# Optimization experiments

Hardware: AMD Instinct MI355X
Metric: run time of the kernel (lower is better)

Reference implementation:

```python
import jax, jax.numpy as jnp
import numpy as np
from jax import lax

N_LINKS = 3000
N_PATHS = 15000
PATH_LEN = 8   # max_len = max(sequences)+1
DL = 16        # link_state_dim
DP = 16        # path_state_dim
RU = 128       # readout_units
OUT = 1
T = 3


def gru_cell(x, h, k, rk, b):
    # keras GRUCell (reset_after=False): kernel [in,3u], recurrent [u,3u], bias [3u]
    gx = x @ k
    gh = h @ rk
    xz, xr, xh = jnp.split(gx, 3, axis=-1)
    hz, hr, hh = jnp.split(gh, 3, axis=-1)
    bz, br, bh = jnp.split(b, 3)
    z = jax.nn.sigmoid(xz + hz + bz)
    r = jax.nn.sigmoid(xr + hr + br)
    c = jnp.tanh(xh + r * hh + bh)
    return z * h + (1.0 - z) * c


def setup_inputs() -> dict:
    key = jax.random.key(0)
    ks = jax.random.split(key, 12)
    s = 0.1
    E = N_PATHS * PATH_LEN
    links = jax.random.randint(ks[0], (E,), 0, N_LINKS, dtype=jnp.int32)
    paths = jnp.repeat(jnp.arange(N_PATHS, dtype=jnp.int32), PATH_LEN)      # sorted, as segment_sum requires
    sequences = jnp.tile(jnp.arange(PATH_LEN, dtype=jnp.int32), N_PATHS)    # position of link on its path
    link_capacity = jax.random.uniform(ks[1], (N_LINKS,), dtype=jnp.float32) * 9.0 + 1.0
    traffic = jax.random.uniform(ks[2], (N_PATHS,), dtype=jnp.float32)
    mask_param = jax.random.normal(ks[3], (N_LINKS, N_PATHS), dtype=jnp.float32) * s  # 'explain_mask'
    path_kernel = jax.random.normal(ks[4], (DL, 3 * DP), dtype=jnp.float32) * s
    path_rec = jax.random.normal(ks[5], (DP, 3 * DP), dtype=jnp.float32) * s
    path_bias = jnp.zeros((3 * DP,), dtype=jnp.float32)
    edge_kernel = jax.random.normal(ks[6], (DP, 3 * DL), dtype=jnp.float32) * s
    edge_rec = jax.random.normal(ks[7], (DL, 3 * DL), dtype=jnp.float32) * s
    edge_bias = jnp.zeros((3 * DL,), dtype=jnp.float32)
    w1 = jax.random.normal(ks[8], (DP, RU), dtype=jnp.float32) * s
    b1 = jnp.zeros((RU,), dtype=jnp.float32)
    w2 = jax.random.normal(ks[9], (RU, RU), dtype=jnp.float32) * s
    b2 = jnp.zeros((RU,), dtype=jnp.float32)
    w3 = jax.random.normal(ks[10], (RU, OUT), dtype=jnp.float32) * s
    b3 = jnp.zeros((OUT,), dtype=jnp.float32)
    return {"links": links, "paths": paths, "sequences": sequences,
            "link_capacity": link_capacity, "traffic": traffic, "mask_param": mask_param,
            "path_kernel": path_kernel, "path_rec": path_rec, "path_bias": path_bias,
            "edge_kernel": edge_kernel, "edge_rec": edge_rec, "edge_bias": edge_bias,
            "w1": w1, "b1": b1, "w2": w2, "b2": b2, "w3": w3, "b3": b3}


def _inner_call(mask, links, paths, sequences, link_capacity, traffic,
                pk, pr, pb, ek, er, eb, w1, b1, w2, b2, w3, b3):
    link_state = jnp.concatenate([link_capacity[:, None], jnp.zeros((N_LINKS, DL - 1))], axis=1)
    path_state = jnp.concatenate([traffic[:, None], jnp.zeros((N_PATHS, DP - 1))], axis=1)
    mask_gathered = mask[links, paths]  # gather_nd -> [E]
    lens = jax.ops.segment_sum(jnp.ones_like(paths), paths, num_segments=N_PATHS)  # [n_paths]
    ts = jnp.arange(PATH_LEN)
    for _ in range(T):
        h_tild = link_state[links] * mask_gathered[:, None]                        # [E, DL]
        # scatter_nd into ragged per-path sequences: [n_paths, max_len, DL]
        link_inputs = jnp.zeros((N_PATHS, PATH_LEN, DL)).at[paths, sequences].add(h_tild)

        def step(h, xt):
            x, t = xt
            hn = gru_cell(x, h, pk, pr, pb)
            valid = (t < lens)[:, None]
            hn = jnp.where(valid, hn, h)               # freeze state past sequence_length
            return hn, jnp.where(valid, hn, 0.0)       # dynamic_rnn zeroes padded outputs

        path_state, outs = lax.scan(step, path_state, (jnp.swapaxes(link_inputs, 0, 1), ts))
        outs = jnp.swapaxes(outs, 0, 1)                # [n_paths, max_len, DP]
        m = outs[paths, sequences]                     # gather_nd -> [E, DP]
        m = jax.ops.segment_sum(m, links, num_segments=N_LINKS)  # unsorted_segment_sum
        link_state = gru_cell(m, link_state, ek, er, eb)
    # readout (dropout inactive at inference)
    h = jax.nn.selu(path_state @ w1 + b1)
    h = jax.nn.selu(h @ w2 + b2)
    r = h @ w3 + b3
    return r, mask_gathered


def reference(links, paths, sequences, link_capacity, traffic, mask_param,
              path_kernel, path_rec, path_bias, edge_kernel, edge_rec, edge_bias,
              w1, b1, w2, b2, w3, b3):
    # scatter_nd of ones over (link, path) ids (duplicates accumulate, as in TF)
    hypergraph = jnp.zeros((N_LINKS, N_PATHS)).at[links, paths].add(1.0)
    mask_inserted = jax.nn.sigmoid(mask_param * hypergraph)
    args = (links, paths, sequences, link_capacity, traffic,
            path_kernel, path_rec, path_bias, edge_kernel, edge_rec, edge_bias,
            w1, b1, w2, b2, w3, b3)
    subgraph_output, subgraph_gathered = _inner_call(mask_inserted, *args)
    model_output, _ = _inner_call(hypergraph, *args)
    return (model_output, subgraph_output, mask_inserted, subgraph_gathered, mask_param)
```

## Files before the change

### kernel.cpp

```cpp
#include <hip/hip_runtime.h>

#define NL 3000
#define NP 15000
#define PLEN 8
#define NE 120000
#define DD 16
#define RU 128

typedef float f4 __attribute__((ext_vector_type(4)));

__device__ __forceinline__ float sigmoidf(float x) { return 1.f / (1.f + __expf(-x)); }
__device__ __forceinline__ float tanh_fast(float x) {
    x = fminf(15.f, fmaxf(-15.f, x));
    float e = __expf(2.f * x);
    return (e - 1.f) / (e + 1.f);
}
__device__ __forceinline__ float seluf(float x) {
    const float scale = 1.0507009873554805f, alpha = 1.6732632423543772f;
    return x > 0.f ? scale * x : scale * alpha * (__expf(x) - 1.f);
}

__global__ __launch_bounds__(256) void k_init(
    const int* __restrict__ links, const int* __restrict__ paths,
    const int* __restrict__ seqs, const float* __restrict__ mp,
    const float* __restrict__ cap, const float* __restrict__ traffic,
    const float* __restrict__ pk,
    float* __restrict__ ls, float* __restrict__ ps, float* __restrict__ magg,
    float* __restrict__ glx, float* __restrict__ mgv,
    int* __restrict__ lens, int* __restrict__ lid, float* __restrict__ out_sg) {
    int tid = blockIdx.x * 256 + threadIdx.x;
    {
        int d = tid & (DD - 1);
        int q = tid >> 4;
        int p = q >= NP ? q - NP : q;
        ps[tid] = (d == 0) ? traffic[p] : 0.f;
    }
    if (tid < 2 * NL * DD) {
        int d = tid & (DD - 1);
        int l = tid >> 4; l = l >= NL ? l - NL : l;
        ls[tid] = (d == 0) ? cap[l] : 0.f;
        magg[tid] = 0.f;
    }
    if (tid < 2 * NL * 48) {
        int c = tid % 48;
        int l = tid / 48; l = l >= NL ? l - NL : l;
        glx[tid] = cap[l] * pk[c];
    }
    if (tid < NP) {
        int p = tid;
        int l8[PLEN], p8[PLEN], s8[PLEN];
#pragma unroll
        for (int j = 0; j < PLEN; ++j) {
            int e = p * PLEN + j;
            l8[j] = links[e]; p8[j] = paths[e]; s8[j] = seqs[e];
        }
        int len = 0;
#pragma unroll
        for (int j = 0; j < PLEN; ++j) len += (p8[j] == p) ? 1 : 0;
        lens[p] = len;
#pragma unroll
        for (int j = 0; j < PLEN; ++j) {
            int e = p * PLEN + j;
            int l = l8[j], s = s8[j];
            int cnt = 0;
#pragma unroll
            for (int k = 0; k < PLEN; ++k)
                cnt += (l8[k] == l && p8[k] == p8[j]) ? 1 : 0;
            float mpv = mp[(size_t)l * NP + p8[j]];
            float sig = sigmoidf(mpv * (float)cnt);
            out_sg[e] = sig;
            lid[p * PLEN + s] = l;
            mgv[p * PLEN + s] = (float)cnt;
            mgv[NP * PLEN + p * PLEN + s] = sig;
        }
    }
}

#define CPY_CHUNK 3750000
template <bool EMIT, int SLICE>
__global__ __launch_bounds__(256) void k_pgru(
    const float* __restrict__ pr, const float* __restrict__ pb,
    const int* __restrict__ lens, const int* __restrict__ lid,
    const float* __restrict__ mgv, const float* __restrict__ glx,
    float* __restrict__ ps, float* __restrict__ magg,
    const f4* __restrict__ mp_in, f4* __restrict__ out_mp, f4* __restrict__ out_mi) {
    int tid = blockIdx.x * 256 + threadIdx.x;
    int j = tid & (DD - 1);
    int idx = tid >> 4;
    int v = idx >= NP ? 1 : 0;
    int pp = idx - v * NP;
    float rz[16], rr[16], rh[16];
#pragma unroll
    for (int k = 0; k < 16; ++k) {
        rz[k] = pr[k * 48 + j];
        rr[k] = pr[k * 48 + 16 + j];
        rh[k] = pr[k * 48 + 32 + j];
    }
    float bz = pb[j], br = pb[16 + j], bh = pb[32 + j];
    float h = ps[tid];
    int len = lens[pp];
    const int* lidp = lid + pp * PLEN;
    const float* mgp = mgv + v * NP * PLEN + pp * PLEN;
#pragma unroll
    for (int s = 0; s < PLEN; ++s) {
        int l = lidp[s];
        float m = mgp[s];
        const float* g = glx + (size_t)(v * NL + l) * 48;
        float gxz = g[j] * m, gxr = g[16 + j] * m, gxh = g[32 + j] * m;
        float ghz = 0.f, ghr = 0.f, ghh = 0.f;
#pragma unroll
        for (int k = 0; k < 16; ++k) {
            float hk = __shfl(h, k, 16);
            ghz = fmaf(hk, rz[k], ghz);
            ghr = fmaf(hk, rr[k], ghr);
            ghh = fmaf(hk, rh[k], ghh);
        }
        float z = sigmoidf(gxz + ghz + bz);
        float r = sigmoidf(gxr + ghr + br);
        float c = tanh_fast(gxh + r * ghh + bh);
        float hn = z * h + (1.f - z) * c;
        if (s < len) {
            h = hn;
            if (EMIT) atomicAdd(&magg[(v * NL + l) * DD + j], hn);
        }
    }
    ps[tid] = h;
    f4 half;
    half.x = 0.5f; half.y = 0.5f; half.z = 0.5f; half.w = 0.5f;
    for (int i = SLICE * CPY_CHUNK + tid; i < (SLICE + 1) * CPY_CHUNK; i += 480000) {
        f4 val = __builtin_nontemporal_load(&mp_in[i]);
        __builtin_nontemporal_store(val, &out_mp[i]);
        __builtin_nontemporal_store(half, &out_mi[i]);
    }
}

__global__ __launch_bounds__(256) void k_link(
    const float* __restrict__ ek, const float* __restrict__ er,
    const float* __restrict__ eb, const float* __restrict__ pk,
    float* __restrict__ magg, float* __restrict__ ls, float* __restrict__ glx) {
    int t = blockIdx.x * 256 + threadIdx.x;
    int j = t & (DD - 1);
    float kz[16], kr[16], kh[16], rz[16], rr[16], rh[16];
#pragma unroll
    for (int k = 0; k < 16; ++k) {
        kz[k] = ek[k * 48 + j];
        kr[k] = ek[k * 48 + 16 + j];
        kh[k] = ek[k * 48 + 32 + j];
        rz[k] = er[k * 48 + j];
        rr[k] = er[k * 48 + 16 + j];
        rh[k] = er[k * 48 + 32 + j];
    }
    float bz = eb[j], br = eb[16 + j], bh = eb[32 + j];
    float x = magg[t];
    magg[t] = 0.f;
    float h = ls[t];
    float gxz = 0.f, gxr = 0.f, gxh = 0.f, ghz = 0.f, ghr = 0.f, ghh = 0.f;
#pragma unroll
    for (int k = 0; k < 16; ++k) {
        float xk = __shfl(x, k, 16);
        float hk = __shfl(h, k, 16);
        gxz = fmaf(xk, kz[k], gxz);
        gxr = fmaf(xk, kr[k], gxr);
        gxh = fmaf(xk, kh[k], gxh);
        ghz = fmaf(hk, rz[k], ghz);
        ghr = fmaf(hk, rr[k], ghr);
        ghh = fmaf(hk, rh[k], ghh);
    }
    float z = sigmoidf(gxz + ghz + bz);
    float r = sigmoidf(gxr + ghr + br);
    float c = tanh_fast(gxh + r * ghh + bh);
    float hn = z * h + (1.f - z) * c;
    ls[t] = hn;
    float gz = 0.f, gr2 = 0.f, gh2 = 0.f;
#pragma unroll
    for (int k = 0; k < 16; ++k) {
        float hk = __shfl(hn, k, 16);
        gz = fmaf(hk, pk[k * 48 + j], gz);
        gr2 = fmaf(hk, pk[k * 48 + 16 + j], gr2);
        gh2 = fmaf(hk, pk[k * 48 + 32 + j], gh2);
    }
    size_t l48 = (size_t)(t >> 4) * 48;
    glx[l48 + j] = gz;
    glx[l48 + 16 + j] = gr2;
    glx[l48 + 32 + j] = gh2;
}

#define PT 32
__global__ __launch_bounds__(256) void k_readout(
    const float* __restrict__ ps,
    const float* __restrict__ w1, const float* __restrict__ b1,
    const float* __restrict__ w2, const float* __restrict__ b2,
    const float* __restrict__ w3, const float* __restrict__ b3,
    float* __restrict__ out,
    const int* __restrict__ links, const int* __restrict__ paths,
    const float* __restrict__ out_sg, float* __restrict__ out_mi) {
    int gtid = blockIdx.x * 256 + threadIdx.x;
    if (gtid < NE)
        out_mi[(size_t)links[gtid] * NP + paths[gtid]] = out_sg[gtid];

    __shared__ float h1s[PT][RU];
    __shared__ float rsum[PT];
    int j = threadIdx.x & (RU - 1);
    int half = threadIdx.x >> 7;
    int pbase = blockIdx.x * PT;
    if (threadIdx.x < PT) rsum[threadIdx.x] = 0.f;
    for (int q = 0; q < PT / 2; ++q) {
        int pl = half * (PT / 2) + q;
        int pg = pbase + pl;
        float acc = b1[j];
        if (pg < 2 * NP) {
            const float* psr = ps + pg * DD;
#pragma unroll
            for (int k = 0; k < DD; ++k) acc = fmaf(psr[k], w1[k * RU + j], acc);
        }
        h1s[pl][j] = seluf(acc);
    }
    __syncthreads();
    float acc2[PT / 2];
#pragma unroll
    for (int q = 0; q < PT / 2; ++q) acc2[q] = b2[j];
    for (int k = 0; k < RU; ++k) {
        float w = w2[k * RU + j];
#pragma unroll
        for (int q = 0; q < PT / 2; ++q)
            acc2[q] = fmaf(h1s[half * (PT / 2) + q][k], w, acc2[q]);
    }
    float w3j = w3[j];
    for (int q = 0; q < PT / 2; ++q) {
        float val = seluf(acc2[q]) * w3j;
#pragma unroll
        for (int off = 32; off > 0; off >>= 1) val += __shfl_down(val, off);
        if ((threadIdx.x & 63) == 0) atomicAdd(&rsum[half * (PT / 2) + q], val);
    }
    __syncthreads();
    if (threadIdx.x < PT) {
        int pg = pbase + threadIdx.x;
        if (pg < 2 * NP) out[pg] = rsum[threadIdx.x] + b3[0];
    }
}

extern "C" void kernel_launch(void* const* d_in, const int* in_sizes, int n_in,
                              void* d_out, int out_size, void* d_ws, size_t ws_size,
                              hipStream_t stream) {
    const int* links = (const int*)d_in[0];
    const int* paths = (const int*)d_in[1];
    const int* seqs = (const int*)d_in[2];
    const float* cap = (const float*)d_in[3];
    const float* traffic = (const float*)d_in[4];
    const float* mask_param = (const float*)d_in[5];
    const float* pk = (const float*)d_in[6];
    const float* pr = (const float*)d_in[7];
    const float* pb = (const float*)d_in[8];
    const float* ek = (const float*)d_in[9];
    const float* er = (const float*)d_in[10];
    const float* eb = (const float*)d_in[11];
    const float* w1 = (const float*)d_in[12];
    const float* b1 = (const float*)d_in[13];
    const float* w2 = (const float*)d_in[14];
    const float* b2 = (const float*)d_in[15];
    const float* w3 = (const float*)d_in[16];
    const float* b3 = (const float*)d_in[17];

    float* out = (float*)d_out;
    float* out_mi = out + 2 * NP;
    float* out_sg = out_mi + (size_t)NL * NP;
    float* out_mp = out_sg + NE;

    char* w = (char*)d_ws;
    float* mgv = (float*)w;  w += (size_t)2 * NP * PLEN * 4;
    float* ls = (float*)w;   w += (size_t)2 * NL * DD * 4;
    float* ps = (float*)w;   w += (size_t)2 * NP * DD * 4;
    float* magg = (float*)w; w += (size_t)2 * NL * DD * 4;
    float* glx = (float*)w;  w += (size_t)2 * NL * 48 * 4;
    int* lens = (int*)w;     w += (size_t)NP * 4;
    int* lid = (int*)w;      w += (size_t)NP * PLEN * 4;

    k_init<<<1875, 256, 0, stream>>>(links, paths, seqs, mask_param, cap, traffic,
                                     pk, ls, ps, magg, glx, mgv, lens, lid, out_sg);
    k_pgru<true, 0><<<1875, 256, 0, stream>>>(pr, pb, lens, lid, mgv, glx, ps, magg,
                                              (const f4*)mask_param, (f4*)out_mp,
                                              (f4*)out_mi);
    k_link<<<375, 256, 0, stream>>>(ek, er, eb, pk, magg, ls, glx);
    k_pgru<true, 1><<<1875, 256, 0, stream>>>(pr, pb, lens, lid, mgv, glx, ps, magg,
                                              (const f4*)mask_param, (f4*)out_mp,
                                              (f4*)out_mi);
    k_link<<<375, 256, 0, stream>>>(ek, er, eb, pk, magg, ls, glx);
    k_pgru<false, 2><<<1875, 256, 0, stream>>>(pr, pb, lens, lid, mgv, glx, ps, magg,
                                               (const f4*)mask_param, (f4*)out_mp,
                                               (f4*)out_mi);
    k_readout<<<(2 * NP + PT - 1) / PT, 256, 0, stream>>>(ps, w1, b1, w2, b2, w3, b3,
                                                          out, links, paths, out_sg,
                                                          out_mi);
}
```

Measured before the change: 633.3 us.

## Fuse init into first path-GRU pass and rebalance the mask copy

Removes the standalone init kernel. Its per-path preprocessing (link ids, duplicate counts, sigmoid mask, lengths) moves into the first path-GRU launch, using shared memory and lane shuffles, and the first step's input gates are computed directly from capacity instead of a precomputed glx table. Zeroing of the workspace uses memset, and a tiny kernel seeds the link state. The big mask_param copy is now split so the last GRU pass only writes the constant 0.5 fill, while the remaining copy moves into the readout kernel. The goal is to cut launch and init overhead and balance memory traffic across kernels, at the cost of more launches via memsets and extra register/shared use in mode 0.

```diff
diff --git a/kernel.cpp b/kernel.cpp
--- a/kernel.cpp
+++ b/kernel.cpp
@@ -9,6 +9,9 @@
 
 typedef float f4 __attribute__((ext_vector_type(4)));
 
+#define N4 ((NL * NP) / 4)
+#define CPY_CHUNK (N4 / 3)
+
 __device__ __forceinline__ float sigmoidf(float x) { return 1.f / (1.f + __expf(-x)); }
 __device__ __forceinline__ float tanh_fast(float x) {
     x = fminf(15.f, fmaxf(-15.f, x));
@@ -20,68 +23,15 @@
     return x > 0.f ? scale * x : scale * alpha * (__expf(x) - 1.f);
 }
 
-__global__ __launch_bounds__(256) void k_init(
+template <int MODE>
+__global__ __launch_bounds__(256) void k_pgru(
     const int* __restrict__ links, const int* __restrict__ paths,
     const int* __restrict__ seqs, const float* __restrict__ mp,
     const float* __restrict__ cap, const float* __restrict__ traffic,
-    const float* __restrict__ pk,
-    float* __restrict__ ls, float* __restrict__ ps, float* __restrict__ magg,
-    float* __restrict__ glx, float* __restrict__ mgv,
-    int* __restrict__ lens, int* __restrict__ lid, float* __restrict__ out_sg) {
-    int tid = blockIdx.x * 256 + threadIdx.x;
-    {
-        int d = tid & (DD - 1);
-        int q = tid >> 4;
-        int p = q >= NP ? q - NP : q;
-        ps[tid] = (d == 0) ? traffic[p] : 0.f;
-    }
-    if (tid < 2 * NL * DD) {
-        int d = tid & (DD - 1);
-        int l = tid >> 4; l = l >= NL ? l - NL : l;
-        ls[tid] = (d == 0) ? cap[l] : 0.f;
-        magg[tid] = 0.f;
-    }
-    if (tid < 2 * NL * 48) {
-        int c = tid % 48;
-        int l = tid / 48; l = l >= NL ? l - NL : l;
-        glx[tid] = cap[l] * pk[c];
-    }
-    if (tid < NP) {
-        int p = tid;
-        int l8[PLEN], p8[PLEN], s8[PLEN];
-#pragma unroll
-        for (int j = 0; j < PLEN; ++j) {
-            int e = p * PLEN + j;
-            l8[j] = links[e]; p8[j] = paths[e]; s8[j] = seqs[e];
-        }
-        int len = 0;
-#pragma unroll
-        for (int j = 0; j < PLEN; ++j) len += (p8[j] == p) ? 1 : 0;
-        lens[p] = len;
-#pragma unroll
-        for (int j = 0; j < PLEN; ++j) {
-            int e = p * PLEN + j;
-            int l = l8[j], s = s8[j];
-            int cnt = 0;
-#pragma unroll
-            for (int k = 0; k < PLEN; ++k)
-                cnt += (l8[k] == l && p8[k] == p8[j]) ? 1 : 0;
-            float mpv = mp[(size_t)l * NP + p8[j]];
-            float sig = sigmoidf(mpv * (float)cnt);
-            out_sg[e] = sig;
-            lid[p * PLEN + s] = l;
-            mgv[p * PLEN + s] = (float)cnt;
-            mgv[NP * PLEN + p * PLEN + s] = sig;
-        }
-    }
-}
-
-#define CPY_CHUNK 3750000
-template <bool EMIT, int SLICE>
-__global__ __launch_bounds__(256) void k_pgru(
-    const float* __restrict__ pr, const float* __restrict__ pb,
-    const int* __restrict__ lens, const int* __restrict__ lid,
-    const float* __restrict__ mgv, const float* __restrict__ glx,
+    const float* __restrict__ pk, const float* __restrict__ pr,
+    const float* __restrict__ pb,
+    int* __restrict__ lens, int* __restrict__ lid, float* __restrict__ mgv,
+    float* __restrict__ out_sg, const float* __restrict__ glx,
     float* __restrict__ ps, float* __restrict__ magg,
     const f4* __restrict__ mp_in, f4* __restrict__ out_mp, f4* __restrict__ out_mi) {
     int tid = blockIdx.x * 256 + threadIdx.x;
@@ -97,16 +47,68 @@
         rh[k] = pr[k * 48 + 32 + j];
     }
     float bz = pb[j], br = pb[16 + j], bh = pb[32 + j];
-    float h = ps[tid];
-    int len = lens[pp];
+
+    __shared__ int s_lid[16][PLEN];
+    __shared__ float s_m[16][PLEN];
+    __shared__ float s_cap[16][PLEN];
+    int g = threadIdx.x >> 4;
+    float h;
+    int len;
+    float pk0z = 0.f, pk0r = 0.f, pk0h = 0.f;
+
+    if (MODE == 0) {
+        pk0z = pk[j]; pk0r = pk[16 + j]; pk0h = pk[32 + j];
+        int l_e = 0, p_e = 0, s_e = 0;
+        if (j < 8) {
+            int e = pp * PLEN + j;
+            l_e = links[e]; p_e = paths[e]; s_e = seqs[e];
+        }
+        int cnt = 0;
+        len = 0;
+#pragma unroll
+        for (int k = 0; k < 8; ++k) {
+            int lk = __shfl(l_e, k, 16);
+            int pk_ = __shfl(p_e, k, 16);
+            cnt += (lk == l_e && pk_ == p_e) ? 1 : 0;
+            len += (pk_ == pp) ? 1 : 0;
+        }
+        if (j < 8) {
+            float capl = cap[l_e];
+            float mpv = mp[(size_t)l_e * NP + p_e];
+            float sig = sigmoidf(mpv * (float)cnt);
+            s_lid[g][s_e] = l_e;
+            s_m[g][s_e] = v ? sig : (float)cnt;
+            s_cap[g][s_e] = capl;
+            if (v == 0) {
+                out_sg[pp * PLEN + j] = sig;
+                lid[pp * PLEN + s_e] = l_e;
+                mgv[pp * PLEN + s_e] = (float)cnt;
+                mgv[NP * PLEN + pp * PLEN + s_e] = sig;
+                if (j == 0) lens[pp] = len;
+            }
+        }
+        h = (j == 0) ? traffic[pp] : 0.f;
+    } else {
+        h = ps[tid];
+        len = lens[pp];
+    }
+
     const int* lidp = lid + pp * PLEN;
     const float* mgp = mgv + v * NP * PLEN + pp * PLEN;
 #pragma unroll
     for (int s = 0; s < PLEN; ++s) {
-        int l = lidp[s];
-        float m = mgp[s];
-        const float* g = glx + (size_t)(v * NL + l) * 48;
-        float gxz = g[j] * m, gxr = g[16 + j] * m, gxh = g[32 + j] * m;
+        int l;
+        float gxz, gxr, gxh;
+        if (MODE == 0) {
+            l = s_lid[g][s];
+            float a = s_cap[g][s] * s_m[g][s];
+            gxz = a * pk0z; gxr = a * pk0r; gxh = a * pk0h;
+        } else {
+            l = lidp[s];
+            float m = mgp[s];
+            const float* gl = glx + (size_t)(v * NL + l) * 48;
+            gxz = gl[j] * m; gxr = gl[16 + j] * m; gxh = gl[32 + j] * m;
+        }
         float ghz = 0.f, ghr = 0.f, ghh = 0.f;
 #pragma unroll
         for (int k = 0; k < 16; ++k) {
@@ -121,16 +123,24 @@
         float hn = z * h + (1.f - z) * c;
         if (s < len) {
             h = hn;
-            if (EMIT) atomicAdd(&magg[(v * NL + l) * DD + j], hn);
+            if (MODE != 2) atomicAdd(&magg[(v * NL + l) * DD + j], hn);
         }
     }
     ps[tid] = h;
+
     f4 half;
     half.x = 0.5f; half.y = 0.5f; half.z = 0.5f; half.w = 0.5f;
-    for (int i = SLICE * CPY_CHUNK + tid; i < (SLICE + 1) * CPY_CHUNK; i += 480000) {
-        f4 val = __builtin_nontemporal_load(&mp_in[i]);
-        __builtin_nontemporal_store(val, &out_mp[i]);
-        __builtin_nontemporal_store(half, &out_mi[i]);
+    if (MODE < 2) {
+        const int lo = MODE * CPY_CHUNK, hi = (MODE + 1) * CPY_CHUNK;
+        for (int i = lo + tid; i < hi; i += 480000) {
+            f4 val = __builtin_nontemporal_load(&mp_in[i]);
+            __builtin_nontemporal_store(val, &out_mp[i]);
+            __builtin_nontemporal_store(half, &out_mi[i]);
+        }
+    } else {
+        for (int i = 2 * CPY_CHUNK + tid; i < N4; i += 480000) {
+            __builtin_nontemporal_store(half, &out_mi[i]);
+        }
     }
 }
 
@@ -193,8 +203,13 @@
     const float* __restrict__ w3, const float* __restrict__ b3,
     float* __restrict__ out,
     const int* __restrict__ links, const int* __restrict__ paths,
-    const float* __restrict__ out_sg, float* __restrict__ out_mi) {
+    const float* __restrict__ out_sg, float* __restrict__ out_mi,
+    const f4* __restrict__ mp_in, f4* __restrict__ out_mp) {
     int gtid = blockIdx.x * 256 + threadIdx.x;
+    for (int i = 2 * CPY_CHUNK + gtid; i < N4; i += 938 * 256) {
+        f4 val = __builtin_nontemporal_load(&mp_in[i]);
+        __builtin_nontemporal_store(val, &out_mp[i]);
+    }
     if (gtid < NE)
         out_mi[(size_t)links[gtid] * NP + paths[gtid]] = out_sg[gtid];
 
@@ -275,20 +290,36 @@
     int* lens = (int*)w;     w += (size_t)NP * 4;
     int* lid = (int*)w;      w += (size_t)NP * PLEN * 4;
 
-    k_init<<<1875, 256, 0, stream>>>(links, paths, seqs, mask_param, cap, traffic,
-                                     pk, ls, ps, magg, glx, mgv, lens, lid, out_sg);
-    k_pgru<true, 0><<<1875, 256, 0, stream>>>(pr, pb, lens, lid, mgv, glx, ps, magg,
-                                              (const f4*)mask_param, (f4*)out_mp,
-                                              (f4*)out_mi);
+    hipMemsetAsync(magg, 0, (size_t)2 * NL * DD * 4, stream);
+    hipMemsetAsync(ls, 0, (size_t)2 * NL * DD * 4, stream);
+    k_pgru<0><<<1875, 256, 0, stream>>>(links, paths, seqs, mask_param, cap, traffic,
+                                        pk, pr, pb, lens, lid, mgv, out_sg, glx,
+                                        ps, magg, (const f4*)mask_param,
+                                        (f4*)out_mp, (f4*)out_mi);
+    {
+        struct LsFix {
+            static __global__ void run(const float* __restrict__ cap,
+                                       float* __restrict__ ls) {
+                int t = blockIdx.x * 256 + threadIdx.x;
+                if (t < 2 * NL) {
+                    int l = t >= NL ? t - NL : t;
+                    ls[t * DD] = cap[l];
+                }
+            }
+        };
+        LsFix::run<<<24, 256, 0, stream>>>(cap, ls);
+    }
     k_link<<<375, 256, 0, stream>>>(ek, er, eb, pk, magg, ls, glx);
-    k_pgru<true, 1><<<1875, 256, 0, stream>>>(pr, pb, lens, lid, mgv, glx, ps, magg,
-                                              (const f4*)mask_param, (f4*)out_mp,
-                                              (f4*)out_mi);
+    k_pgru<1><<<1875, 256, 0, stream>>>(links, paths, seqs, mask_param, cap, traffic,
+                                        pk, pr, pb, lens, lid, mgv, out_sg, glx,
+                                        ps, magg, (const f4*)mask_param,
+                                        (f4*)out_mp, (f4*)out_mi);
     k_link<<<375, 256, 0, stream>>>(ek, er, eb, pk, magg, ls, glx);
-    k_pgru<false, 2><<<1875, 256, 0, stream>>>(pr, pb, lens, lid, mgv, glx, ps, magg,
-                                               (const f4*)mask_param, (f4*)out_mp,
-                                               (f4*)out_mi);
-    k_readout<<<(2 * NP + PT - 1) / PT, 256, 0, stream>>>(ps, w1, b1, w2, b2, w3, b3,
-                                                          out, links, paths, out_sg,
-                                                          out_mi);
-}
+    k_pgru<2><<<1875, 256, 0, stream>>>(links, paths, seqs, mask_param, cap, traffic,
+                                        pk, pr, pb, lens, lid, mgv, out_sg, glx,
+                                        ps, magg, (const f4*)mask_param,
+                                        (f4*)out_mp, (f4*)out_mi);
+    k_readout<<<938, 256, 0, stream>>>(ps, w1, b1, w2, b2, w3, b3, out, links, paths,
+                                       out_sg, out_mi, (const f4*)mask_param,
+                                       (f4*)out_mp);
+}
```

Result: faster. 614.7 us (-2.9%).
